# Kernel tuning notes

Hardware: AMD Instinct MI355X
Metric: run time of the kernel (lower is better)

Reference implementation:

```python
import jax, jax.numpy as jnp
import numpy as np

K = 3          # kernel size
SH, SW = 2, 1  # stride
PH, PW = 1, 1  # padding


def conv2d(x, w, b, stride, pad):
    y = jax.lax.conv_general_dilated(
        x, w, window_strides=stride,
        padding=[(pad[0], pad[0]), (pad[1], pad[1])],
        dimension_numbers=('NCHW', 'OIHW', 'NCHW'))
    return y + b[None, :, None, None]


def setup_inputs() -> dict:
    key = jax.random.key(0)
    ks = jax.random.split(key, 4)
    x = jax.random.normal(ks[0], (8, 64, 128, 128), jnp.float32)
    # scale offset weights small so sampled offsets are O(1) pixels (exercises
    # the bilinear path without sampling far out of bounds)
    w_offset = jax.random.normal(ks[1], (18, 64, 3, 3), jnp.float32) * 0.02
    b_offset = jnp.zeros((18,), jnp.float32)
    w_mask = jax.random.normal(ks[2], (9, 64, 3, 3), jnp.float32) * 0.05
    b_mask = jnp.zeros((9,), jnp.float32)
    w_conv = jax.random.normal(ks[3], (64, 64, 3, 3), jnp.float32) * (1.0 / 24.0)
    return dict(x=x, w_offset=w_offset, b_offset=b_offset,
                w_mask=w_mask, b_mask=b_mask, w_conv=w_conv)


def _bilinear_gather(x, py, px):
    # x: [B,C,H,W]; py, px: [B,K2,Ho,Wo] float sampling coordinates.
    # Zero-padding outside the image (torchvision deform_conv2d semantics).
    B, C, H, W = x.shape
    y0f = jnp.floor(py)
    x0f = jnp.floor(px)
    dy = py - y0f
    dx = px - x0f
    y0 = y0f.astype(jnp.int32)
    x0 = x0f.astype(jnp.int32)

    def corner(yi, xi, wgt):
        valid = (yi >= 0) & (yi < H) & (xi >= 0) & (xi < W)
        yc = jnp.clip(yi, 0, H - 1)
        xc = jnp.clip(xi, 0, W - 1)
        # per-batch fancy gather -> [B, C, K2, Ho, Wo]
        g = jax.vmap(lambda xb, yb, xbi: xb[:, yb, xbi])(x, yc, xc)
        return g * (wgt * valid)[:, None]

    return (corner(y0,     x0,     (1 - dy) * (1 - dx))
            + corner(y0,     x0 + 1, (1 - dy) * dx)
            + corner(y0 + 1, x0,     dy * (1 - dx))
            + corner(y0 + 1, x0 + 1, dy * dx))


def reference(x, w_offset, b_offset, w_mask, b_mask, w_conv):
    B, C, H, W = x.shape
    offset = conv2d(x, w_offset, b_offset, (SH, SW), (PH, PW))   # [B, 2*K2, Ho, Wo]
    mask = jax.nn.sigmoid(conv2d(x, w_mask, b_mask, (SH, SW), (PH, PW)))  # [B, K2, Ho, Wo]
    Ho, Wo = offset.shape[2], offset.shape[3]
    K2 = K * K
    off = offset.reshape(B, K2, 2, Ho, Wo)
    off_y = off[:, :, 0]   # [B,K2,Ho,Wo]
    off_x = off[:, :, 1]
    ky = (jnp.arange(K2) // K).astype(jnp.float32)
    kx = (jnp.arange(K2) % K).astype(jnp.float32)
    hs = (jnp.arange(Ho) * SH - PH).astype(jnp.float32)
    ws = (jnp.arange(Wo) * SW - PW).astype(jnp.float32)
    py = off_y + ky[None, :, None, None] + hs[None, None, :, None]
    px = off_x + kx[None, :, None, None] + ws[None, None, None, :]
    sampled = _bilinear_gather(x, py, px) * mask[:, None]  # [B,C,K2,Ho,Wo]
    # weighted accumulate over in-channels and kernel taps
    out = jnp.einsum('ock,bckhw->bohw', w_conv.reshape(-1, C, K2), sampled)
    return out
```

## Files before the change

### kernel.cpp

```cpp
#include <hip/hip_runtime.h>
#include <hip/hip_bf16.h>
#include <hip/hip_fp16.h>
#include <math.h>

#define BB 8
#define CC 64
#define HH 128
#define WW 128
#define HO 64
#define WO 128
#define OC 64
#define HW (HH * WW)
#define HOWO (HO * WO)
#define NPM (BB * 9 * HOWO)

typedef __attribute__((ext_vector_type(8))) short short8;
typedef __attribute__((ext_vector_type(4))) float floatx4;

union BfBits { __hip_bfloat16 h; unsigned short s; };

__device__ __forceinline__ float bf2f(unsigned short u) {
    return __uint_as_float(((unsigned int)u) << 16);
}
__device__ __forceinline__ unsigned short f2bf(float f) {
    BfBits b; b.h = __float2bfloat16(f); return b.s;
}

__global__ __launch_bounds__(256) void transpose_x(
    const float* __restrict__ x, unsigned short* __restrict__ xT)
{
    __shared__ float T[64][65];
    int tid = threadIdx.x;
    int bx = blockIdx.x;
    int b = bx & 7;
    int rest = bx >> 3;
    int y = rest >> 1;
    int w0 = (rest & 1) * 64;

    int wl = tid & 63;
    int grp = tid >> 6;
#pragma unroll
    for (int i = 0; i < 16; ++i) {
        int c = grp * 16 + i;
        T[c][wl] = x[(((size_t)b * CC + c) * HH + y) * WW + w0 + wl];
    }
    __syncthreads();
    int c = tid & 63;
#pragma unroll
    for (int i = 0; i < 16; ++i) {
        int wp = grp * 16 + i;
        xT[(((size_t)b * HH + y) * WW + (w0 + wp)) * 64 + c] = f2bf(T[c][wp]);
    }
}

__global__ __launch_bounds__(256) void make_wom(
    const float* __restrict__ w_off, const float* __restrict__ w_msk,
    unsigned short* __restrict__ Wom)
{
    int i = blockIdx.x * 256 + threadIdx.x;
    if (i >= 32 * 576) return;
    int ch = i / 576;
    int kk = i % 576;
    int xs = kk >> 6;
    int c = kk & 63;
    float v = 0.0f;
    if (ch < 18)      v = w_off[(ch * CC + c) * 9 + xs];
    else if (ch < 27) v = w_msk[((ch - 18) * CC + c) * 9 + xs];
    Wom[i] = f2bf(v);
}

__global__ __launch_bounds__(256) void make_w2(
    const float* __restrict__ w_conv, unsigned short* __restrict__ W2)
{
    int i = blockIdx.x * 256 + threadIdx.x;
    int k = i % 9;
    int c = (i / 9) % CC;
    int o = i / (CC * 9);
    W2[((size_t)k * OC + o) * CC + c] = f2bf(w_conv[i]);
}

__global__ __launch_bounds__(256) void om_gemm(
    const unsigned short* __restrict__ xT, const unsigned short* __restrict__ Wom,
    const float* __restrict__ b_off, const float* __restrict__ b_msk,
    uint2* __restrict__ CFH, unsigned int* __restrict__ CFP)
{
    __shared__ __align__(16) unsigned short Xs[3][34][72];
    __shared__ float omr[27][33];

    int tid = threadIdx.x;
    int bx = blockIdx.x;
    int b = bx & 7;
    int rest = bx >> 3;
    int h = rest >> 2;
    int w0 = (rest & 3) * 32;
    int h2 = 2 * h - 1;

    for (int u = tid; u < 816; u += 256) {
        int ky = u / 272;
        int rem = u - ky * 272;
        int col = rem >> 3;
        int cb = rem & 7;
        int hy = h2 + ky;
        int wc = w0 - 1 + col;
        short8 v = {0, 0, 0, 0, 0, 0, 0, 0};
        if ((unsigned)hy < (unsigned)HH && (unsigned)wc < (unsigned)WW) {
            v = *(const short8*)(xT + (((size_t)b * HH + hy) * WW + wc) * 64 + cb * 8);
        }
        *(short8*)&Xs[ky][col][cb * 8] = v;
    }
    __syncthreads();

    int lane = tid & 63;
    int wv = __builtin_amdgcn_readfirstlane(tid >> 6);
    int mt = wv & 1;
    int nt = wv >> 1;
    int m16 = lane & 15;
    int q = lane >> 4;

    floatx4 acc = (floatx4){0.f, 0.f, 0.f, 0.f};
    const unsigned short* wa = Wom + (mt * 16 + m16) * 576 + q * 8;
#pragma unroll
    for (int t = 0; t < 18; ++t) {
        const int xs = t >> 1;
        const int ky = xs / 3, kx = xs % 3;
        short8 af = *(const short8*)(wa + t * 32);
        short8 bf = *(const short8*)&Xs[ky][nt * 16 + m16 + kx][(t & 1) * 32 + q * 8];
        acc = __builtin_amdgcn_mfma_f32_16x16x32_bf16(af, bf, acc, 0, 0, 0);
    }
#pragma unroll
    for (int r = 0; r < 4; ++r) {
        int ch = mt * 16 + q * 4 + r;
        if (ch < 27) omr[ch][nt * 16 + m16] = acc[r];
    }
    __syncthreads();

    for (int u = tid; u < 288; u += 256) {
        int kk = u >> 5;
        int pos = u & 31;
        float offy = omr[2 * kk][pos] + b_off[2 * kk];
        float offx = omr[2 * kk + 1][pos] + b_off[2 * kk + 1];
        float mk = 1.0f / (1.0f + __expf(-(omr[18 + kk][pos] + b_msk[kk])));
        float py = offy + (float)(kk / 3) + (float)h2;
        float px = offx + (float)(kk % 3) + (float)(w0 + pos - 1);

        float y0f = floorf(py), x0f = floorf(px);
        float dy = py - y0f, dx = px - x0f;
        int y0 = (int)y0f, x0 = (int)x0f;
        int y1 = y0 + 1, x1 = x0 + 1;
        bool vy0 = (unsigned)y0 < (unsigned)HH;
        bool vy1 = (unsigned)y1 < (unsigned)HH;
        bool vx0 = (unsigned)x0 < (unsigned)WW;
        bool vx1 = (unsigned)x1 < (unsigned)WW;
        float w00 = (1.0f - dy) * (1.0f - dx) * ((vy0 && vx0) ? mk : 0.0f);
        float w01 = (1.0f - dy) * dx          * ((vy0 && vx1) ? mk : 0.0f);
        float w10 = dy * (1.0f - dx)          * ((vy1 && vx0) ? mk : 0.0f);
        float w11 = dy * dx                   * ((vy1 && vx1) ? mk : 0.0f);
        int xbase = min(max(x0, 0), WW - 2);
        bool s0 = x0 > xbase;
        bool s1 = x1 > xbase;
        float cxA = (s0 ? 0.f : w00) + (s1 ? 0.f : w01);
        float cyA = (s0 ? w00 : 0.f) + (s1 ? w01 : 0.f);
        float cxB = (s0 ? 0.f : w10) + (s1 ? 0.f : w11);
        float cyB = (s0 ? w10 : 0.f) + (s1 ? w11 : 0.f);
        int yc0 = min(max(y0, 0), HH - 1);
        int yc1 = min(max(y1, 0), HH - 1);
        unsigned int r0 = (unsigned)(yc0 * WW + xbase);
        unsigned int r1 = (unsigned)(yc1 * WW + xbase);

        int idx = ((b * 9 + kk) * HO + h) * WO + w0 + pos;
        __half2 hA = __floats2half2_rn(cxA, cyA);
        __half2 hB = __floats2half2_rn(cxB, cyB);
        uint2 hv;
        hv.x = *reinterpret_cast<unsigned int*>(&hA);
        hv.y = *reinterpret_cast<unsigned int*>(&hB);
        CFH[idx] = hv;
        CFP[idx] = r0 | (r1 << 14);
    }
}

__global__ __launch_bounds__(256) void dconv_mfma(
    const unsigned short* __restrict__ xT,
    const uint2* __restrict__ CFH, const unsigned int* __restrict__ CFP,
    const unsigned short* __restrict__ W2,
    float* __restrict__ out)
{
    __shared__ __align__(16) unsigned short S[2][32][64];

    int tid = threadIdx.x;
    int lane = tid & 63;
    int wv = __builtin_amdgcn_readfirstlane(tid >> 6);

    int bx = blockIdx.x;
    int b = bx & 7;
    int rest = bx >> 3;
    int h = rest >> 2;
    int w0 = (rest & 3) * 32;

    int c = lane;
    int p0 = wv * 8;
    const int m16 = lane & 15;
    const int q = lane >> 4;

    floatx4 acc[2];
    acc[0] = (floatx4){0.f, 0.f, 0.f, 0.f};
    acc[1] = (floatx4){0.f, 0.f, 0.f, 0.f};

    const unsigned short* xTb = xT + (size_t)b * HW * 64;
    int cfb = ((b * 9) * HO + h) * WO + w0 + p0;

    unsigned short U[8][4];
    float4 c4[8];

    auto issue = [&](int k) {
#pragma unroll
        for (int i = 0; i < 8; ++i) {
            int idx = cfb + k * HOWO + i;
            uint2 hv = CFH[idx];
            __half2 hA = *reinterpret_cast<__half2*>(&hv.x);
            __half2 hB = *reinterpret_cast<__half2*>(&hv.y);
            c4[i].x = __low2float(hA);
            c4[i].y = __high2float(hA);
            c4[i].z = __low2float(hB);
            c4[i].w = __high2float(hB);
            unsigned int pk = CFP[idx];
            unsigned int r0 = pk & 0x3FFFu;
            unsigned int r1 = pk >> 14;
            const unsigned short* pA = xTb + (size_t)r0 * 64 + c;
            const unsigned short* pB = xTb + (size_t)r1 * 64 + c;
            U[i][0] = pA[0];
            U[i][1] = pA[64];
            U[i][2] = pB[0];
            U[i][3] = pB[64];
        }
    };
    auto combine_store = [&](int buf) {
#pragma unroll
        for (int i = 0; i < 8; ++i) {
            float v = c4[i].x * bf2f(U[i][0]) + c4[i].y * bf2f(U[i][1])
                    + c4[i].z * bf2f(U[i][2]) + c4[i].w * bf2f(U[i][3]);
            int pos = p0 + i;
            S[buf][pos][((c >> 3) ^ (pos & 7)) * 8 + (c & 7)] = f2bf(v);
        }
    };

    issue(0);
    combine_store(0);

#pragma unroll
    for (int k = 0; k < 9; ++k) {
        __syncthreads();
        if (k < 8) issue(k + 1);
        {
            const unsigned short* wk = W2 + ((size_t)(k * OC) + wv * 16 + m16) * CC + q * 8;
            int buf = k & 1;
#pragma unroll
            for (int s = 0; s < 2; ++s) {
                short8 af = *(const short8*)(wk + s * 32);
                int cb = ((q + 4 * s) ^ (m16 & 7)) * 8;
                short8 bf0 = *(const short8*)&S[buf][m16][cb];
                short8 bf1 = *(const short8*)&S[buf][16 + m16][cb];
                acc[0] = __builtin_amdgcn_mfma_f32_16x16x32_bf16(af, bf0, acc[0], 0, 0, 0);
                acc[1] = __builtin_amdgcn_mfma_f32_16x16x32_bf16(af, bf1, acc[1], 0, 0, 0);
            }
        }
        if (k < 8) combine_store((k + 1) & 1);
    }

#pragma unroll
    for (int nt = 0; nt < 2; ++nt) {
#pragma unroll
        for (int r = 0; r < 4; ++r) {
            int o = wv * 16 + q * 4 + r;
            out[(((size_t)b * OC + o) * HO + h) * WO + w0 + nt * 16 + m16]
                = acc[nt][r];
        }
    }
}

extern "C" void kernel_launch(void* const* d_in, const int* in_sizes, int n_in,
                              void* d_out, int out_size, void* d_ws, size_t ws_size,
                              hipStream_t stream)
{
    const float* x      = (const float*)d_in[0];
    const float* w_off  = (const float*)d_in[1];
    const float* b_off  = (const float*)d_in[2];
    const float* w_msk  = (const float*)d_in[3];
    const float* b_msk  = (const float*)d_in[4];
    const float* w_conv = (const float*)d_in[5];
    float* out = (float*)d_out;

    uint2* CFH = (uint2*)d_ws;
    unsigned int* CFP = (unsigned int*)(CFH + NPM);
    unsigned short* xT = (unsigned short*)(CFP + NPM);
    unsigned short* W2 = xT + (size_t)BB * HW * 64;
    unsigned short* Wom = W2 + 9 * OC * CC;

    transpose_x<<<dim3(2048), dim3(256), 0, stream>>>(x, xT);
    make_wom<<<dim3(72), dim3(256), 0, stream>>>(w_off, w_msk, Wom);
    make_w2<<<dim3(144), dim3(256), 0, stream>>>(w_conv, W2);
    om_gemm<<<dim3(2048), dim3(256), 0, stream>>>(xT, Wom, b_off, b_msk, CFH, CFP);
    dconv_mfma<<<dim3(2048), dim3(256), 0, stream>>>(xT, CFH, CFP, W2, out);
}
```

Baseline: 152.4 us.

## Fuse offset/mask GEMM into deformable conv and pre-pair adjacent pixels

```diff
diff --git a/kernel.cpp b/kernel.cpp
--- a/kernel.cpp
+++ b/kernel.cpp
@@ -12,131 +12,122 @@
 #define OC 64
 #define HW (HH * WW)
 #define HOWO (HO * WO)
-#define NPM (BB * 9 * HOWO)
 
 typedef __attribute__((ext_vector_type(8))) short short8;
 typedef __attribute__((ext_vector_type(4))) float floatx4;
 
 union BfBits { __hip_bfloat16 h; unsigned short s; };
-
-__device__ __forceinline__ float bf2f(unsigned short u) {
-    return __uint_as_float(((unsigned int)u) << 16);
-}
 __device__ __forceinline__ unsigned short f2bf(float f) {
     BfBits b; b.h = __float2bfloat16(f); return b.s;
 }
-
-__global__ __launch_bounds__(256) void transpose_x(
-    const float* __restrict__ x, unsigned short* __restrict__ xT)
+__device__ __forceinline__ float bflo(unsigned int u) {
+    return __uint_as_float(u << 16);
+}
+__device__ __forceinline__ float bfhi(unsigned int u) {
+    return __uint_as_float(u & 0xFFFF0000u);
+}
+
+__global__ __launch_bounds__(256) void prep(
+    const float* __restrict__ x,
+    const float* __restrict__ w_off, const float* __restrict__ w_msk,
+    const float* __restrict__ w_conv,
+    unsigned short* __restrict__ xT, unsigned int* __restrict__ xP,
+    unsigned short* __restrict__ Wom, unsigned short* __restrict__ W2)
 {
-    __shared__ float T[64][65];
+    __shared__ float T[64][130];
     int tid = threadIdx.x;
     int bx = blockIdx.x;
-    int b = bx & 7;
-    int rest = bx >> 3;
-    int y = rest >> 1;
-    int w0 = (rest & 1) * 64;
-
-    int wl = tid & 63;
-    int grp = tid >> 6;
-#pragma unroll
-    for (int i = 0; i < 16; ++i) {
-        int c = grp * 16 + i;
-        T[c][wl] = x[(((size_t)b * CC + c) * HH + y) * WW + w0 + wl];
-    }
-    __syncthreads();
-    int c = tid & 63;
-#pragma unroll
-    for (int i = 0; i < 16; ++i) {
-        int wp = grp * 16 + i;
-        xT[(((size_t)b * HH + y) * WW + (w0 + wp)) * 64 + c] = f2bf(T[c][wp]);
-    }
-}
-
-__global__ __launch_bounds__(256) void make_wom(
-    const float* __restrict__ w_off, const float* __restrict__ w_msk,
-    unsigned short* __restrict__ Wom)
+    if (bx < 1024) {
+        int b = bx & 7, y = bx >> 3;
+        int wl = tid & 127, c0 = tid >> 7;
+#pragma unroll
+        for (int i = 0; i < 32; ++i) {
+            int c = 2 * i + c0;
+            T[c][wl] = x[(((size_t)b * CC + c) * HH + y) * WW + wl];
+        }
+        __syncthreads();
+        int c = tid & 63, wg = tid >> 6;
+#pragma unroll
+        for (int i = 0; i < 32; ++i) {
+            int wp = wg * 32 + i;
+            unsigned int lo = f2bf(T[c][wp]);
+            unsigned int hi = (wp < 127) ? f2bf(T[c][wp + 1]) : 0u;
+            size_t e = (((size_t)b * HH + y) * WW + wp) * 64 + c;
+            xT[e] = (unsigned short)lo;
+            xP[e] = lo | (hi << 16);
+        }
+    } else if (bx < 1096) {
+        int i = (bx - 1024) * 256 + tid;
+        int ch = i / 576, kk = i % 576;
+        int xs = kk >> 6, c = kk & 63;
+        float v = 0.0f;
+        if (ch < 18)      v = w_off[(ch * CC + c) * 9 + xs];
+        else if (ch < 27) v = w_msk[((ch - 18) * CC + c) * 9 + xs];
+        Wom[i] = f2bf(v);
+    } else {
+        int i = (bx - 1096) * 256 + tid;
+        int k = i % 9, c = (i / 9) % CC, o = i / (CC * 9);
+        W2[((size_t)k * OC + o) * CC + c] = f2bf(w_conv[i]);
+    }
+}
+
+__global__ __launch_bounds__(256) void fused(
+    const unsigned short* __restrict__ xT, const unsigned int* __restrict__ xP,
+    const unsigned short* __restrict__ Wom, const unsigned short* __restrict__ W2,
+    const float* __restrict__ b_off, const float* __restrict__ b_msk,
+    float* __restrict__ out)
 {
-    int i = blockIdx.x * 256 + threadIdx.x;
-    if (i >= 32 * 576) return;
-    int ch = i / 576;
-    int kk = i % 576;
-    int xs = kk >> 6;
-    int c = kk & 63;
-    float v = 0.0f;
-    if (ch < 18)      v = w_off[(ch * CC + c) * 9 + xs];
-    else if (ch < 27) v = w_msk[((ch - 18) * CC + c) * 9 + xs];
-    Wom[i] = f2bf(v);
-}
-
-__global__ __launch_bounds__(256) void make_w2(
-    const float* __restrict__ w_conv, unsigned short* __restrict__ W2)
-{
-    int i = blockIdx.x * 256 + threadIdx.x;
-    int k = i % 9;
-    int c = (i / 9) % CC;
-    int o = i / (CC * 9);
-    W2[((size_t)k * OC + o) * CC + c] = f2bf(w_conv[i]);
-}
-
-__global__ __launch_bounds__(256) void om_gemm(
-    const unsigned short* __restrict__ xT, const unsigned short* __restrict__ Wom,
-    const float* __restrict__ b_off, const float* __restrict__ b_msk,
-    uint2* __restrict__ CFH, unsigned int* __restrict__ CFP)
-{
-    __shared__ __align__(16) unsigned short Xs[3][34][72];
-    __shared__ float omr[27][33];
+    __shared__ __align__(16) char lds[18304];
+    typedef unsigned short XsRow[34][72];
+    XsRow* Xs = (XsRow*)lds;
+    unsigned short (*S)[32][64] = (unsigned short(*)[32][64])lds;
+    uint4* meta = (uint4*)(lds + 8192);
+    float (*omr)[33] = (float(*)[33])(lds + 14720);
 
     int tid = threadIdx.x;
+    int lane = tid & 63;
+    int wv = __builtin_amdgcn_readfirstlane(tid >> 6);
     int bx = blockIdx.x;
     int b = bx & 7;
     int rest = bx >> 3;
     int h = rest >> 2;
     int w0 = (rest & 3) * 32;
     int h2 = 2 * h - 1;
+    int m16 = lane & 15, q = lane >> 4;
 
     for (int u = tid; u < 816; u += 256) {
         int ky = u / 272;
         int rem = u - ky * 272;
-        int col = rem >> 3;
-        int cb = rem & 7;
-        int hy = h2 + ky;
-        int wc = w0 - 1 + col;
+        int col = rem >> 3, cb = rem & 7;
+        int hy = h2 + ky, wc = w0 - 1 + col;
         short8 v = {0, 0, 0, 0, 0, 0, 0, 0};
-        if ((unsigned)hy < (unsigned)HH && (unsigned)wc < (unsigned)WW) {
+        if ((unsigned)hy < (unsigned)HH && (unsigned)wc < (unsigned)WW)
             v = *(const short8*)(xT + (((size_t)b * HH + hy) * WW + wc) * 64 + cb * 8);
-        }
         *(short8*)&Xs[ky][col][cb * 8] = v;
     }
     __syncthreads();
 
-    int lane = tid & 63;
-    int wv = __builtin_amdgcn_readfirstlane(tid >> 6);
-    int mt = wv & 1;
-    int nt = wv >> 1;
-    int m16 = lane & 15;
-    int q = lane >> 4;
-
-    floatx4 acc = (floatx4){0.f, 0.f, 0.f, 0.f};
-    const unsigned short* wa = Wom + (mt * 16 + m16) * 576 + q * 8;
-#pragma unroll
-    for (int t = 0; t < 18; ++t) {
-        const int xs = t >> 1;
-        const int ky = xs / 3, kx = xs % 3;
-        short8 af = *(const short8*)(wa + t * 32);
-        short8 bf = *(const short8*)&Xs[ky][nt * 16 + m16 + kx][(t & 1) * 32 + q * 8];
-        acc = __builtin_amdgcn_mfma_f32_16x16x32_bf16(af, bf, acc, 0, 0, 0);
-    }
-#pragma unroll
-    for (int r = 0; r < 4; ++r) {
-        int ch = mt * 16 + q * 4 + r;
-        if (ch < 27) omr[ch][nt * 16 + m16] = acc[r];
+    {
+        int mt = wv & 1, nt = wv >> 1;
+        floatx4 a = (floatx4){0.f, 0.f, 0.f, 0.f};
+        const unsigned short* wa = Wom + (mt * 16 + m16) * 576 + q * 8;
+#pragma unroll
+        for (int t = 0; t < 18; ++t) {
+            int xs = t >> 1, ky = xs / 3, kx = xs % 3;
+            short8 af = *(const short8*)(wa + t * 32);
+            short8 bf = *(const short8*)&Xs[ky][nt * 16 + m16 + kx][(t & 1) * 32 + q * 8];
+            a = __builtin_amdgcn_mfma_f32_16x16x32_bf16(af, bf, a, 0, 0, 0);
+        }
+#pragma unroll
+        for (int r = 0; r < 4; ++r) {
+            int ch = mt * 16 + q * 4 + r;
+            if (ch < 27) omr[ch][nt * 16 + m16] = a[r];
+        }
     }
     __syncthreads();
 
     for (int u = tid; u < 288; u += 256) {
-        int kk = u >> 5;
-        int pos = u & 31;
+        int kk = u >> 5, pos = u & 31;
         float offy = omr[2 * kk][pos] + b_off[2 * kk];
         float offx = omr[2 * kk + 1][pos] + b_off[2 * kk + 1];
         float mk = 1.0f / (1.0f + __expf(-(omr[18 + kk][pos] + b_msk[kk])));
@@ -164,87 +155,49 @@
         float cyB = (s0 ? w10 : 0.f) + (s1 ? w11 : 0.f);
         int yc0 = min(max(y0, 0), HH - 1);
         int yc1 = min(max(y1, 0), HH - 1);
-        unsigned int r0 = (unsigned)(yc0 * WW + xbase);
-        unsigned int r1 = (unsigned)(yc1 * WW + xbase);
-
-        int idx = ((b * 9 + kk) * HO + h) * WO + w0 + pos;
+
         __half2 hA = __floats2half2_rn(cxA, cyA);
         __half2 hB = __floats2half2_rn(cxB, cyB);
-        uint2 hv;
-        hv.x = *reinterpret_cast<unsigned int*>(&hA);
-        hv.y = *reinterpret_cast<unsigned int*>(&hB);
-        CFH[idx] = hv;
-        CFP[idx] = r0 | (r1 << 14);
-    }
-}
-
-__global__ __launch_bounds__(256) void dconv_mfma(
-    const unsigned short* __restrict__ xT,
-    const uint2* __restrict__ CFH, const unsigned int* __restrict__ CFP,
-    const unsigned short* __restrict__ W2,
-    float* __restrict__ out)
-{
-    __shared__ __align__(16) unsigned short S[2][32][64];
-
-    int tid = threadIdx.x;
-    int lane = tid & 63;
-    int wv = __builtin_amdgcn_readfirstlane(tid >> 6);
-
-    int bx = blockIdx.x;
-    int b = bx & 7;
-    int rest = bx >> 3;
-    int h = rest >> 2;
-    int w0 = (rest & 3) * 32;
-
+        uint4 mu;
+        mu.x = __builtin_bit_cast(unsigned int, hA);
+        mu.y = __builtin_bit_cast(unsigned int, hB);
+        mu.z = (unsigned)(yc0 * WW + xbase) * 256u;
+        mu.w = (unsigned)(yc1 * WW + xbase) * 256u;
+        meta[u] = mu;
+    }
+    __syncthreads();
+
+    int p0 = wv * 8;
     int c = lane;
-    int p0 = wv * 8;
-    const int m16 = lane & 15;
-    const int q = lane >> 4;
-
-    floatx4 acc[2];
-    acc[0] = (floatx4){0.f, 0.f, 0.f, 0.f};
-    acc[1] = (floatx4){0.f, 0.f, 0.f, 0.f};
-
-    const unsigned short* xTb = xT + (size_t)b * HW * 64;
-    int cfb = ((b * 9) * HO + h) * WO + w0 + p0;
-
-    unsigned short U[8][4];
-    float4 c4[8];
+    const char* xPb = (const char*)(xP + (size_t)b * HW * 64);
+    floatx4 acc0 = (floatx4){0.f, 0.f, 0.f, 0.f};
+    floatx4 acc1 = (floatx4){0.f, 0.f, 0.f, 0.f};
+
+    uint4 M[8];
+    unsigned int G0[8], G1[8];
 
     auto issue = [&](int k) {
 #pragma unroll
         for (int i = 0; i < 8; ++i) {
-            int idx = cfb + k * HOWO + i;
-            uint2 hv = CFH[idx];
-            __half2 hA = *reinterpret_cast<__half2*>(&hv.x);
-            __half2 hB = *reinterpret_cast<__half2*>(&hv.y);
-            c4[i].x = __low2float(hA);
-            c4[i].y = __high2float(hA);
-            c4[i].z = __low2float(hB);
-            c4[i].w = __high2float(hB);
-            unsigned int pk = CFP[idx];
-            unsigned int r0 = pk & 0x3FFFu;
-            unsigned int r1 = pk >> 14;
-            const unsigned short* pA = xTb + (size_t)r0 * 64 + c;
-            const unsigned short* pB = xTb + (size_t)r1 * 64 + c;
-            U[i][0] = pA[0];
-            U[i][1] = pA[64];
-            U[i][2] = pB[0];
-            U[i][3] = pB[64];
+            M[i] = meta[k * 32 + p0 + i];
+            G0[i] = *(const unsigned int*)(xPb + M[i].z + 4 * c);
+            G1[i] = *(const unsigned int*)(xPb + M[i].w + 4 * c);
         }
     };
-    auto combine_store = [&](int buf) {
+    auto store = [&](int buf) {
 #pragma unroll
         for (int i = 0; i < 8; ++i) {
-            float v = c4[i].x * bf2f(U[i][0]) + c4[i].y * bf2f(U[i][1])
-                    + c4[i].z * bf2f(U[i][2]) + c4[i].w * bf2f(U[i][3]);
+            __half2 hA = __builtin_bit_cast(__half2, M[i].x);
+            __half2 hB = __builtin_bit_cast(__half2, M[i].y);
+            float v = __low2float(hA) * bflo(G0[i]) + __high2float(hA) * bfhi(G0[i])
+                    + __low2float(hB) * bflo(G1[i]) + __high2float(hB) * bfhi(G1[i]);
             int pos = p0 + i;
             S[buf][pos][((c >> 3) ^ (pos & 7)) * 8 + (c & 7)] = f2bf(v);
         }
     };
 
     issue(0);
-    combine_store(0);
+    store(0);
 
 #pragma unroll
     for (int k = 0; k < 9; ++k) {
@@ -259,20 +212,20 @@
                 int cb = ((q + 4 * s) ^ (m16 & 7)) * 8;
                 short8 bf0 = *(const short8*)&S[buf][m16][cb];
                 short8 bf1 = *(const short8*)&S[buf][16 + m16][cb];
-                acc[0] = __builtin_amdgcn_mfma_f32_16x16x32_bf16(af, bf0, acc[0], 0, 0, 0);
-                acc[1] = __builtin_amdgcn_mfma_f32_16x16x32_bf16(af, bf1, acc[1], 0, 0, 0);
+                acc0 = __builtin_amdgcn_mfma_f32_16x16x32_bf16(af, bf0, acc0, 0, 0, 0);
+                acc1 = __builtin_amdgcn_mfma_f32_16x16x32_bf16(af, bf1, acc1, 0, 0, 0);
             }
         }
-        if (k < 8) combine_store((k + 1) & 1);
+        if (k < 8) store((k + 1) & 1);
     }
 
 #pragma unroll
     for (int nt = 0; nt < 2; ++nt) {
+        floatx4 av = nt ? acc1 : acc0;
 #pragma unroll
         for (int r = 0; r < 4; ++r) {
             int o = wv * 16 + q * 4 + r;
-            out[(((size_t)b * OC + o) * HO + h) * WO + w0 + nt * 16 + m16]
-                = acc[nt][r];
+            out[(((size_t)b * OC + o) * HO + h) * WO + w0 + nt * 16 + m16] = av[r];
         }
     }
 }
@@ -289,15 +242,13 @@
     const float* w_conv = (const float*)d_in[5];
     float* out = (float*)d_out;
 
-    uint2* CFH = (uint2*)d_ws;
-    unsigned int* CFP = (unsigned int*)(CFH + NPM);
-    unsigned short* xT = (unsigned short*)(CFP + NPM);
-    unsigned short* W2 = xT + (size_t)BB * HW * 64;
-    unsigned short* Wom = W2 + 9 * OC * CC;
-
-    transpose_x<<<dim3(2048), dim3(256), 0, stream>>>(x, xT);
-    make_wom<<<dim3(72), dim3(256), 0, stream>>>(w_off, w_msk, Wom);
-    make_w2<<<dim3(144), dim3(256), 0, stream>>>(w_conv, W2);
-    om_gemm<<<dim3(2048), dim3(256), 0, stream>>>(xT, Wom, b_off, b_msk, CFH, CFP);
-    dconv_mfma<<<dim3(2048), dim3(256), 0, stream>>>(xT, CFH, CFP, W2, out);
-}
+    unsigned short* xT = (unsigned short*)d_ws;
+    unsigned int* xP = (unsigned int*)(xT + (size_t)BB * HW * 64);
+    unsigned short* Wom = (unsigned short*)(xP + (size_t)BB * HW * 64);
+    unsigned short* W2 = Wom + 32 * 576;
+
+    prep<<<dim3(1240), dim3(256), 0, stream>>>(x, w_off, w_msk, w_conv,
+                                               xT, xP, Wom, W2);
+    fused<<<dim3(2048), dim3(256), 0, stream>>>(xT, xP, Wom, W2,
+                                                b_off, b_msk, out);
+}
```

New measurement: 144.5 us. 1.05x faster.
